# Optimization experiments

Hardware: AMD Instinct MI355X
Metric: run time of the kernel (lower is better)

The kernel has to match this reference:

```python
import jax, jax.numpy as jnp
import numpy as np

N_ITERS = 1000   # n_iters default
LR = 0.1         # SGD lr default (schedule_lr=False -> constant lr)
EPS = 1e-8       # eps in LogMagTargetFrequencyLoss


def setup_inputs() -> dict:
    key = jax.random.key(0)
    k1, k2 = jax.random.split(key)
    # random log-magnitude target in dB (scaled to plausible dB range)
    target_dB = jax.random.normal(k1, (512,), dtype=jnp.float32) * 6.0
    # matches torch.rand(1, 16, 6) init of self.coefs / self.sos
    sos_init = jax.random.uniform(k2, (1, 16, 6), dtype=jnp.float32)
    return {"target_dB": target_dB, "sos_init": sos_init}


def _log_mag_loss(sos, target):
    """LogMagTargetFrequencyLoss: MSE between 20*log10|H(e^jw)| of the SOS
    cascade and the target dB response. sos: (1,16,6); target: (1,N)."""
    n = target.shape[-1]
    w = jnp.linspace(0.0, jnp.pi, n)                      # frequency grid (N,)
    zm = jnp.exp(-1j * w.astype(jnp.complex64))            # z^-1 on unit circle
    powers = jnp.stack([jnp.ones_like(zm), zm, zm * zm])   # (3, N): [1, z^-1, z^-2]
    b = sos[..., :3].astype(jnp.complex64)                 # (1,16,3)
    a = sos[..., 3:].astype(jnp.complex64)                 # (1,16,3)
    num = jnp.einsum('bsc,cn->bsn', b, powers)             # (1,16,N)
    den = jnp.einsum('bsc,cn->bsn', a, powers)             # (1,16,N)
    h = jnp.prod(num / den, axis=1)                        # cascade product -> (1,N)
    mag = 20.0 * jnp.log10(jnp.abs(h) + EPS)
    return jnp.mean((mag - target) ** 2)


def reference(target_dB, sos_init):
    target = target_dB.reshape(1, -1)
    grad_fn = jax.grad(_log_mag_loss)

    def step(sos, _):
        g = grad_fn(sos, target)
        return sos - LR * g, None   # plain SGD, constant lr (schedule_lr=False)

    sos, _ = jax.lax.scan(step, sos_init, None, length=N_ITERS)
    # pole_zero=False: out_sos aliases self.sos, so the returned tensor is the
    # post-step (final optimized) coefficients.
    return sos
```

## Files before the change

kernel.cpp:

```cpp
#include <hip/hip_runtime.h>
#include <math.h>

#define NITER 1000
#define LRATE 0.1f

typedef unsigned int v2u __attribute__((ext_vector_type(2)));

__device__ __forceinline__ float rcpf(float x) { return __builtin_amdgcn_rcpf(x); }

__device__ __forceinline__ float readlane_f(float v, int l) {
    return __int_as_float(__builtin_amdgcn_readlane(__float_as_int(v), l));
}

template<int CTRL>
__device__ __forceinline__ float dpp_mov(float v) {
    return __int_as_float(__builtin_amdgcn_update_dpp(0, __float_as_int(v), CTRL, 0xF, 0xF, true));
}

__device__ __forceinline__ int lane_id() {
    return __builtin_amdgcn_mbcnt_hi(~0u, __builtin_amdgcn_mbcnt_lo(~0u, 0u));
}

__device__ __forceinline__ void swap16(float& x, float& y) {
#if __has_builtin(__builtin_amdgcn_permlane16_swap)
    v2u r = __builtin_amdgcn_permlane16_swap(__float_as_uint(x), __float_as_uint(y), false, false);
    x = __uint_as_float(r[0]);
    y = __uint_as_float(r[1]);
#else
    const bool up = lane_id() & 16;
    const float send = up ? x : y;
    const float recv = __shfl_xor(send, 16);
    x = up ? recv : x;
    y = up ? y : recv;
#endif
}

__device__ __forceinline__ void swap32(float& x, float& y) {
#if __has_builtin(__builtin_amdgcn_permlane32_swap)
    v2u r = __builtin_amdgcn_permlane32_swap(__float_as_uint(x), __float_as_uint(y), false, false);
    x = __uint_as_float(r[0]);
    y = __uint_as_float(r[1]);
#else
    const bool up = lane_id() & 32;
    const float send = up ? x : y;
    const float recv = __shfl_xor(send, 32);
    x = up ? recv : x;
    y = up ? y : recv;
#endif
}

__global__ __launch_bounds__(1024, 1)
void sgd_filter_design_kernel(const float* __restrict__ target,
                              const float* __restrict__ sos_init,
                              float* __restrict__ out)
{
    const int t = threadIdx.x;
    const int w = t >> 6;
    const int L = t & 63;

    __shared__ __align__(16) float wq[16][576];
    __shared__ __align__(16) float Kbuf[576];

    const float PI = 3.14159265358979323846f;
    float C1[8], S1[8], C2[8], S2[8];
    #pragma unroll
    for (int f = 0; f < 8; ++f) {
        const int n = 8 * L + f;
        const float wr = PI * (float)n / 511.0f;
        const float c1 = cosf(wr), s1 = sinf(wr);
        C1[f] = c1; S1[f] = s1;
        C2[f] = 2.0f * c1 * c1 - 1.0f;
        S2[f] = 2.0f * s1 * c1;
    }

    float mKt = 0.0f;
    int kaddr = 0;
    if (t < 512) {
        mKt = -0.03392925639869154f * target[t];
        kaddr = 8 * (t >> 3) + 4 * (t >> 5) + (t & 7);
    }

    const int sw = 8 * L + 4 * (L >> 2);
    const int col = ((L & 16) >> 2) | ((L & 32) >> 4) | (L & 1);
    const bool up1 = L & 1;

    float v0 = 0.0f;
    if (col < 6) v0 = sos_init[6 * w + col];
    float B0f = readlane_f(v0, 0);
    float B1f = readlane_f(v0, 1);
    float B2f = readlane_f(v0, 32);
    float A0f = readlane_f(v0, 33);
    float A1f = readlane_f(v0, 16);
    float A2f = readlane_f(v0, 17);

    for (int it = 0; it < NITER; ++it) {
        float imn[8], imd[8], qs[8];
        #pragma unroll
        for (int f = 0; f < 8; ++f) {
            const float nr = fmaf(B2f, C2[f], fmaf(B1f, C1[f], B0f));
            const float ni = fmaf(B2f, S2[f], B1f * S1[f]);
            const float dr = fmaf(A2f, C2[f], fmaf(A1f, C1[f], A0f));
            const float di = fmaf(A2f, S2[f], A1f * S1[f]);
            const float mn = fmaf(nr, nr, ni * ni);
            const float md = fmaf(dr, dr, di * di);
            const float rr = rcpf(mn * md);
            const float iimd = rr * mn;
            const float iimn = rr * md;
            qs[f] = mn * iimd;
            imn[f] = iimn;
            imd[f] = iimd;
        }
        {
            const float4 q0 = {qs[0], qs[1], qs[2], qs[3]};
            const float4 q1 = {qs[4], qs[5], qs[6], qs[7]};
            *reinterpret_cast<float4*>(&wq[w][sw])     = q0;
            *reinterpret_cast<float4*>(&wq[w][sw + 4]) = q1;
        }
        __syncthreads();

        if (t < 512) {
            float p[16];
            #pragma unroll
            for (int ww = 0; ww < 16; ++ww) p[ww] = wq[ww][kaddr];
            p[0] *= p[8];  p[1] *= p[9];  p[2] *= p[10]; p[3] *= p[11];
            p[4] *= p[12]; p[5] *= p[13]; p[6] *= p[14]; p[7] *= p[15];
            p[0] *= p[4];  p[1] *= p[5];  p[2] *= p[6];  p[3] *= p[7];
            p[0] *= p[2];  p[1] *= p[3];
            p[0] *= p[1];
            Kbuf[kaddr] = fmaf(__log2f(p[0]), 0.10213724040f, mKt);
        }
        __syncthreads();

        const float4 k0 = *reinterpret_cast<const float4*>(&Kbuf[sw]);
        const float4 k1 = *reinterpret_cast<const float4*>(&Kbuf[sw + 4]);
        const float Kf[8] = {k0.x, k0.y, k0.z, k0.w, k1.x, k1.y, k1.z, k1.w};

        float X0, X1, X2, X3, X4, X5;
        #pragma unroll
        for (int f = 0; f < 8; ++f) {
            const float E = Kf[f] * imn[f];
            const float F = Kf[f] * imd[f];
            if (f == 0) {
                X0 = E;            X3 = F;
                X1 = E * C1[f];    X4 = F * C1[f];
                X2 = E * C2[f];    X5 = F * C2[f];
            } else {
                X0 += E;                      X3 += F;
                X1 = fmaf(E, C1[f], X1);      X4 = fmaf(F, C1[f], X4);
                X2 = fmaf(E, C2[f], X2);      X5 = fmaf(F, C2[f], X5);
            }
        }
        const float g6[6] = {X0, X1, X2, X3, X4, X5};

        float r4v[4];
        #pragma unroll
        for (int i = 0; i < 4; ++i) {
            float x = g6[i];
            float y = (i + 4 < 6) ? g6[i + 4] : 0.0f;
            swap16(x, y);
            r4v[i] = x + y;
        }
        float r2v[2];
        #pragma unroll
        for (int i = 0; i < 2; ++i) {
            float x = r4v[i], y = r4v[i + 2];
            swap32(x, y);
            r2v[i] = x + y;
        }
        float r1v;
        {
            const float x = r2v[0], y = r2v[1];
            const float P = up1 ? y : x, Q = up1 ? x : y;
            r1v = P + dpp_mov<0xB1>(Q);
        }
        r1v += dpp_mov<0x4E>(r1v);
        r1v += dpp_mov<0x128>(r1v);
        r1v += __shfl_xor(r1v, 4);

        const float S0 = readlane_f(r1v, 0);
        const float S1v = readlane_f(r1v, 1);
        const float S2v = readlane_f(r1v, 32);
        const float T0 = readlane_f(r1v, 33);
        const float T1v = readlane_f(r1v, 16);
        const float T2v = readlane_f(r1v, 17);

        const float gb0 = fmaf(B0f, S0, fmaf(B1f, S1v, B2f * S2v));
        const float gb1 = fmaf(B0f + B2f, S1v, B1f * S0);
        const float gb2 = fmaf(B0f, S2v, fmaf(B1f, S1v, B2f * S0));
        const float ga0 = fmaf(A0f, T0, fmaf(A1f, T1v, A2f * T2v));
        const float ga1 = fmaf(A0f + A2f, T1v, A1f * T0);
        const float ga2 = fmaf(A0f, T2v, fmaf(A1f, T1v, A2f * T0));

        B0f = fmaf(-LRATE, gb0, B0f);
        B1f = fmaf(-LRATE, gb1, B1f);
        B2f = fmaf(-LRATE, gb2, B2f);
        A0f = fmaf( LRATE, ga0, A0f);
        A1f = fmaf( LRATE, ga1, A1f);
        A2f = fmaf( LRATE, ga2, A2f);
    }

    if (L == 0) {
        out[6 * w + 0] = B0f;
        out[6 * w + 1] = B1f;
        out[6 * w + 2] = B2f;
        out[6 * w + 3] = A0f;
        out[6 * w + 4] = A1f;
        out[6 * w + 5] = A2f;
    }
}

extern "C" void kernel_launch(void* const* d_in, const int* in_sizes, int n_in,
                              void* d_out, int out_size, void* d_ws, size_t ws_size,
                              hipStream_t stream) {
    const float* target   = (const float*)d_in[0];
    const float* sos_init = (const float*)d_in[1];
    float* out = (float*)d_out;
    hipLaunchKernelGGL(sgd_filter_design_kernel, dim3(1), dim3(1024), 0, stream,
                       target, sos_init, out);
}
```

Measured before the change: 1.479 ms.

## Split cascade product across all 1024 threads and store K in fp16

The per-frequency product over 16 sections is now split between lane pairs: each thread multiplies 8 sections and a DPP swap combines the pair, so all 1024 threads take part instead of 512. The loss-gradient factor K is written to shared memory as fp16 with a linear index, so each lane reads its 8 values with a single 16-byte load. The q writes are also interleaved with the computation in two halves. The intent is a shorter critical path per iteration, but K loses precision in fp16, which may change the optimized coefficients over 1000 iterations.

```diff
diff --git a/kernel.cpp b/kernel.cpp
--- a/kernel.cpp
+++ b/kernel.cpp
@@ -59,7 +59,7 @@
     const int L = t & 63;
 
     __shared__ __align__(16) float wq[16][576];
-    __shared__ __align__(16) float Kbuf[576];
+    __shared__ __align__(16) __fp16 Kh[512];
 
     const float PI = 3.14159265358979323846f;
     float C1[8], S1[8], C2[8], S2[8];
@@ -73,12 +73,10 @@
         S2[f] = 2.0f * s1 * c1;
     }
 
-    float mKt = 0.0f;
-    int kaddr = 0;
-    if (t < 512) {
-        mKt = -0.03392925639869154f * target[t];
-        kaddr = 8 * (t >> 3) + 4 * (t >> 5) + (t & 7);
-    }
+    const int fK = t >> 1;
+    const float mKt = -0.03392925639869154f * target[fK];
+    const int kaddr = 8 * (fK >> 3) + 4 * (fK >> 5) + (fK & 7);
+    const int wbase = (L & 1) ? 8 : 0;
 
     const int sw = 8 * L + 4 * (L >> 2);
     const int col = ((L & 16) >> 2) | ((L & 32) >> 4) | (L & 1);
@@ -94,46 +92,59 @@
     float A2f = readlane_f(v0, 17);
 
     for (int it = 0; it < NITER; ++it) {
-        float imn[8], imd[8], qs[8];
-        #pragma unroll
-        for (int f = 0; f < 8; ++f) {
-            const float nr = fmaf(B2f, C2[f], fmaf(B1f, C1[f], B0f));
-            const float ni = fmaf(B2f, S2[f], B1f * S1[f]);
-            const float dr = fmaf(A2f, C2[f], fmaf(A1f, C1[f], A0f));
-            const float di = fmaf(A2f, S2[f], A1f * S1[f]);
-            const float mn = fmaf(nr, nr, ni * ni);
-            const float md = fmaf(dr, dr, di * di);
-            const float rr = rcpf(mn * md);
-            const float iimd = rr * mn;
-            const float iimn = rr * md;
-            qs[f] = mn * iimd;
-            imn[f] = iimn;
-            imd[f] = iimd;
-        }
+        float imn[8], imd[8];
+        #pragma unroll
+        for (int half = 0; half < 2; ++half) {
+            float4 qv;
+            #pragma unroll
+            for (int j = 0; j < 4; ++j) {
+                const int f = 4 * half + j;
+                const float nr = fmaf(B2f, C2[f], fmaf(B1f, C1[f], B0f));
+                const float ni = fmaf(B2f, S2[f], B1f * S1[f]);
+                const float dr = fmaf(A2f, C2[f], fmaf(A1f, C1[f], A0f));
+                const float di = fmaf(A2f, S2[f], A1f * S1[f]);
+                const float mn = fmaf(nr, nr, ni * ni);
+                const float md = fmaf(dr, dr, di * di);
+                const float rr = rcpf(mn * md);
+                const float iimd = rr * mn;
+                const float iimn = rr * md;
+                imn[f] = iimn;
+                imd[f] = iimd;
+                const float q = mn * iimd;
+                if (j == 0) qv.x = q;
+                else if (j == 1) qv.y = q;
+                else if (j == 2) qv.z = q;
+                else qv.w = q;
+            }
+            *reinterpret_cast<float4*>(&wq[w][sw + 4 * half]) = qv;
+        }
+        __syncthreads();
+
         {
-            const float4 q0 = {qs[0], qs[1], qs[2], qs[3]};
-            const float4 q1 = {qs[4], qs[5], qs[6], qs[7]};
-            *reinterpret_cast<float4*>(&wq[w][sw])     = q0;
-            *reinterpret_cast<float4*>(&wq[w][sw + 4]) = q1;
+            float p0 = wq[wbase + 0][kaddr];
+            float p1 = wq[wbase + 1][kaddr];
+            float p2 = wq[wbase + 2][kaddr];
+            float p3 = wq[wbase + 3][kaddr];
+            const float p4 = wq[wbase + 4][kaddr];
+            const float p5 = wq[wbase + 5][kaddr];
+            const float p6 = wq[wbase + 6][kaddr];
+            const float p7 = wq[wbase + 7][kaddr];
+            p0 *= p4; p1 *= p5; p2 *= p6; p3 *= p7;
+            p0 *= p2; p1 *= p3;
+            p0 *= p1;
+            const float ptot = p0 * dpp_mov<0xB1>(p0);
+            const float Kv = fmaf(__log2f(ptot), 0.10213724040f, mKt);
+            if (!(L & 1)) Kh[fK] = (__fp16)Kv;
         }
         __syncthreads();
 
-        if (t < 512) {
-            float p[16];
+        float Kf[8];
+        {
+            union { uint4 u; __fp16 h[8]; } kc;
+            kc.u = *reinterpret_cast<const uint4*>(&Kh[8 * L]);
             #pragma unroll
-            for (int ww = 0; ww < 16; ++ww) p[ww] = wq[ww][kaddr];
-            p[0] *= p[8];  p[1] *= p[9];  p[2] *= p[10]; p[3] *= p[11];
-            p[4] *= p[12]; p[5] *= p[13]; p[6] *= p[14]; p[7] *= p[15];
-            p[0] *= p[4];  p[1] *= p[5];  p[2] *= p[6];  p[3] *= p[7];
-            p[0] *= p[2];  p[1] *= p[3];
-            p[0] *= p[1];
-            Kbuf[kaddr] = fmaf(__log2f(p[0]), 0.10213724040f, mKt);
-        }
-        __syncthreads();
-
-        const float4 k0 = *reinterpret_cast<const float4*>(&Kbuf[sw]);
-        const float4 k1 = *reinterpret_cast<const float4*>(&Kbuf[sw + 4]);
-        const float Kf[8] = {k0.x, k0.y, k0.z, k0.w, k1.x, k1.y, k1.z, k1.w};
+            for (int f = 0; f < 8; ++f) Kf[f] = (float)kc.h[f];
+        }
 
         float X0, X1, X2, X3, X4, X5;
         #pragma unroll
```

After: 1.991 ms. 1.35x slower.

## Pack two SOS sections per wave and use real-polynomial squared magnitudes

Applied to the files above, without the earlier changes.

The squared magnitudes |N|^2 and |D|^2 are now computed as real cosine polynomials (P0 + P1 cos w + P2 cos 2w) from per-section coefficients, so the complex evaluation and the sine tables go away. Each wave now handles two biquad sections, which halves the block to 512 threads and 8 waves. The cross-wave product reduction uses 8 instead of 16 loads, and all threads take part. This cuts barrier participants and per-iteration ALU work, at the cost of more registers per thread and a clamp with fmaxf that slightly changes numerics near zeros.

```diff
diff --git a/kernel.cpp b/kernel.cpp
--- a/kernel.cpp
+++ b/kernel.cpp
@@ -49,7 +49,7 @@
 #endif
 }
 
-__global__ __launch_bounds__(1024, 1)
+__global__ __launch_bounds__(512, 1)
 void sgd_filter_design_kernel(const float* __restrict__ target,
                               const float* __restrict__ sos_init,
                               float* __restrict__ out)
@@ -58,57 +58,72 @@
     const int w = t >> 6;
     const int L = t & 63;
 
-    __shared__ __align__(16) float wq[16][576];
+    __shared__ __align__(16) float wq[8][576];
     __shared__ __align__(16) float Kbuf[576];
 
     const float PI = 3.14159265358979323846f;
-    float C1[8], S1[8], C2[8], S2[8];
+    float C1[8], C2[8];
     #pragma unroll
     for (int f = 0; f < 8; ++f) {
         const int n = 8 * L + f;
         const float wr = PI * (float)n / 511.0f;
-        const float c1 = cosf(wr), s1 = sinf(wr);
-        C1[f] = c1; S1[f] = s1;
+        const float c1 = cosf(wr);
+        C1[f] = c1;
         C2[f] = 2.0f * c1 * c1 - 1.0f;
-        S2[f] = 2.0f * s1 * c1;
     }
 
-    float mKt = 0.0f;
-    int kaddr = 0;
-    if (t < 512) {
-        mKt = -0.03392925639869154f * target[t];
-        kaddr = 8 * (t >> 3) + 4 * (t >> 5) + (t & 7);
-    }
-
+    const float mKt = -0.03392925639869154f * target[t];
+    const int kaddr = 8 * (t >> 3) + 4 * (t >> 5) + (t & 7);
     const int sw = 8 * L + 4 * (L >> 2);
-    const int col = ((L & 16) >> 2) | ((L & 32) >> 4) | (L & 1);
-    const bool up1 = L & 1;
+
+    const int col = ((L & 16) >> 1) | ((L & 32) >> 3) | ((L & 1) << 1) | ((L & 2) >> 1);
+    const bool up1 = L & 1, up2 = L & 2;
 
     float v0 = 0.0f;
-    if (col < 6) v0 = sos_init[6 * w + col];
-    float B0f = readlane_f(v0, 0);
-    float B1f = readlane_f(v0, 1);
-    float B2f = readlane_f(v0, 32);
-    float A0f = readlane_f(v0, 33);
-    float A1f = readlane_f(v0, 16);
-    float A2f = readlane_f(v0, 17);
+    if (col < 12) v0 = sos_init[12 * w + col];
+    float b0A = readlane_f(v0, 0);
+    float b1A = readlane_f(v0, 2);
+    float b2A = readlane_f(v0, 1);
+    float a0A = readlane_f(v0, 3);
+    float a1A = readlane_f(v0, 32);
+    float a2A = readlane_f(v0, 34);
+    float b0B = readlane_f(v0, 33);
+    float b1B = readlane_f(v0, 35);
+    float b2B = readlane_f(v0, 16);
+    float a0B = readlane_f(v0, 18);
+    float a1B = readlane_f(v0, 17);
+    float a2B = readlane_f(v0, 19);
 
     for (int it = 0; it < NITER; ++it) {
-        float imn[8], imd[8], qs[8];
+        const float PA0 = fmaf(b0A, b0A, fmaf(b1A, b1A, b2A * b2A));
+        const float PA1 = 2.0f * b1A * (b0A + b2A);
+        const float PA2 = 2.0f * b0A * b2A;
+        const float QA0 = fmaf(a0A, a0A, fmaf(a1A, a1A, a2A * a2A));
+        const float QA1 = 2.0f * a1A * (a0A + a2A);
+        const float QA2 = 2.0f * a0A * a2A;
+        const float PB0 = fmaf(b0B, b0B, fmaf(b1B, b1B, b2B * b2B));
+        const float PB1 = 2.0f * b1B * (b0B + b2B);
+        const float PB2 = 2.0f * b0B * b2B;
+        const float QB0 = fmaf(a0B, a0B, fmaf(a1B, a1B, a2B * a2B));
+        const float QB1 = 2.0f * a1B * (a0B + a2B);
+        const float QB2 = 2.0f * a0B * a2B;
+
+        float imnA[8], imdA[8], imnB[8], imdB[8], qs[8];
         #pragma unroll
         for (int f = 0; f < 8; ++f) {
-            const float nr = fmaf(B2f, C2[f], fmaf(B1f, C1[f], B0f));
-            const float ni = fmaf(B2f, S2[f], B1f * S1[f]);
-            const float dr = fmaf(A2f, C2[f], fmaf(A1f, C1[f], A0f));
-            const float di = fmaf(A2f, S2[f], A1f * S1[f]);
-            const float mn = fmaf(nr, nr, ni * ni);
-            const float md = fmaf(dr, dr, di * di);
-            const float rr = rcpf(mn * md);
-            const float iimd = rr * mn;
-            const float iimn = rr * md;
-            qs[f] = mn * iimd;
-            imn[f] = iimn;
-            imd[f] = iimd;
+            float mnA = fmaf(PA2, C2[f], fmaf(PA1, C1[f], PA0));
+            float mdA = fmaf(QA2, C2[f], fmaf(QA1, C1[f], QA0));
+            float mnB = fmaf(PB2, C2[f], fmaf(PB1, C1[f], PB0));
+            float mdB = fmaf(QB2, C2[f], fmaf(QB1, C1[f], QB0));
+            mnA = fmaxf(mnA, 1e-18f);
+            mdA = fmaxf(mdA, 1e-18f);
+            mnB = fmaxf(mnB, 1e-18f);
+            mdB = fmaxf(mdB, 1e-18f);
+            const float rA = rcpf(mnA * mdA);
+            const float rB = rcpf(mnB * mdB);
+            imnA[f] = rA * mdA; imdA[f] = rA * mnA;
+            imnB[f] = rB * mdB; imdB[f] = rB * mnB;
+            qs[f] = (mnA * imdA[f]) * (mnB * imdB[f]);
         }
         {
             const float4 q0 = {qs[0], qs[1], qs[2], qs[3]};
@@ -118,16 +133,15 @@
         }
         __syncthreads();
 
-        if (t < 512) {
-            float p[16];
-            #pragma unroll
-            for (int ww = 0; ww < 16; ++ww) p[ww] = wq[ww][kaddr];
-            p[0] *= p[8];  p[1] *= p[9];  p[2] *= p[10]; p[3] *= p[11];
-            p[4] *= p[12]; p[5] *= p[13]; p[6] *= p[14]; p[7] *= p[15];
-            p[0] *= p[4];  p[1] *= p[5];  p[2] *= p[6];  p[3] *= p[7];
-            p[0] *= p[2];  p[1] *= p[3];
-            p[0] *= p[1];
-            Kbuf[kaddr] = fmaf(__log2f(p[0]), 0.10213724040f, mKt);
+        {
+            float p0 = wq[0][kaddr], p1 = wq[1][kaddr];
+            float p2 = wq[2][kaddr], p3 = wq[3][kaddr];
+            const float p4 = wq[4][kaddr], p5 = wq[5][kaddr];
+            const float p6 = wq[6][kaddr], p7 = wq[7][kaddr];
+            p0 *= p4; p1 *= p5; p2 *= p6; p3 *= p7;
+            p0 *= p2; p1 *= p3;
+            p0 *= p1;
+            Kbuf[kaddr] = fmaf(__log2f(p0), 0.10213724040f, mKt);
         }
         __syncthreads();
 
@@ -135,77 +149,117 @@
         const float4 k1 = *reinterpret_cast<const float4*>(&Kbuf[sw + 4]);
         const float Kf[8] = {k0.x, k0.y, k0.z, k0.w, k1.x, k1.y, k1.z, k1.w};
 
-        float X0, X1, X2, X3, X4, X5;
+        float SA0, SA1, SA2, TA0, TA1, TA2;
+        float SB0, SB1, SB2, TB0, TB1, TB2;
         #pragma unroll
         for (int f = 0; f < 8; ++f) {
-            const float E = Kf[f] * imn[f];
-            const float F = Kf[f] * imd[f];
+            const float EA = Kf[f] * imnA[f];
+            const float FA = Kf[f] * imdA[f];
+            const float EB = Kf[f] * imnB[f];
+            const float FB = Kf[f] * imdB[f];
             if (f == 0) {
-                X0 = E;            X3 = F;
-                X1 = E * C1[f];    X4 = F * C1[f];
-                X2 = E * C2[f];    X5 = F * C2[f];
+                SA0 = EA;          TA0 = FA;
+                SA1 = EA * C1[f];  TA1 = FA * C1[f];
+                SA2 = EA * C2[f];  TA2 = FA * C2[f];
+                SB0 = EB;          TB0 = FB;
+                SB1 = EB * C1[f];  TB1 = FB * C1[f];
+                SB2 = EB * C2[f];  TB2 = FB * C2[f];
             } else {
-                X0 += E;                      X3 += F;
-                X1 = fmaf(E, C1[f], X1);      X4 = fmaf(F, C1[f], X4);
-                X2 = fmaf(E, C2[f], X2);      X5 = fmaf(F, C2[f], X5);
+                SA0 += EA;                    TA0 += FA;
+                SA1 = fmaf(EA, C1[f], SA1);   TA1 = fmaf(FA, C1[f], TA1);
+                SA2 = fmaf(EA, C2[f], SA2);   TA2 = fmaf(FA, C2[f], TA2);
+                SB0 += EB;                    TB0 += FB;
+                SB1 = fmaf(EB, C1[f], SB1);   TB1 = fmaf(FB, C1[f], TB1);
+                SB2 = fmaf(EB, C2[f], SB2);   TB2 = fmaf(FB, C2[f], TB2);
             }
         }
-        const float g6[6] = {X0, X1, X2, X3, X4, X5};
-
+        const float g12[12] = {SA0, SA1, SA2, TA0, TA1, TA2,
+                               SB0, SB1, SB2, TB0, TB1, TB2};
+
+        float r8v[8];
+        #pragma unroll
+        for (int i = 0; i < 8; ++i) {
+            float x = g12[i];
+            float y = (i + 8 < 12) ? g12[i + 8] : 0.0f;
+            swap16(x, y);
+            r8v[i] = x + y;
+        }
         float r4v[4];
         #pragma unroll
         for (int i = 0; i < 4; ++i) {
-            float x = g6[i];
-            float y = (i + 4 < 6) ? g6[i + 4] : 0.0f;
-            swap16(x, y);
+            float x = r8v[i], y = r8v[i + 4];
+            swap32(x, y);
             r4v[i] = x + y;
         }
         float r2v[2];
         #pragma unroll
         for (int i = 0; i < 2; ++i) {
-            float x = r4v[i], y = r4v[i + 2];
-            swap32(x, y);
-            r2v[i] = x + y;
+            const float x = r4v[i], y = r4v[i + 2];
+            const float P = up1 ? y : x, Q = up1 ? x : y;
+            r2v[i] = P + dpp_mov<0xB1>(Q);
         }
         float r1v;
         {
             const float x = r2v[0], y = r2v[1];
-            const float P = up1 ? y : x, Q = up1 ? x : y;
-            r1v = P + dpp_mov<0xB1>(Q);
-        }
-        r1v += dpp_mov<0x4E>(r1v);
+            const float P = up2 ? y : x, Q = up2 ? x : y;
+            r1v = P + dpp_mov<0x4E>(Q);
+        }
         r1v += dpp_mov<0x128>(r1v);
         r1v += __shfl_xor(r1v, 4);
 
-        const float S0 = readlane_f(r1v, 0);
-        const float S1v = readlane_f(r1v, 1);
-        const float S2v = readlane_f(r1v, 32);
-        const float T0 = readlane_f(r1v, 33);
-        const float T1v = readlane_f(r1v, 16);
-        const float T2v = readlane_f(r1v, 17);
-
-        const float gb0 = fmaf(B0f, S0, fmaf(B1f, S1v, B2f * S2v));
-        const float gb1 = fmaf(B0f + B2f, S1v, B1f * S0);
-        const float gb2 = fmaf(B0f, S2v, fmaf(B1f, S1v, B2f * S0));
-        const float ga0 = fmaf(A0f, T0, fmaf(A1f, T1v, A2f * T2v));
-        const float ga1 = fmaf(A0f + A2f, T1v, A1f * T0);
-        const float ga2 = fmaf(A0f, T2v, fmaf(A1f, T1v, A2f * T0));
-
-        B0f = fmaf(-LRATE, gb0, B0f);
-        B1f = fmaf(-LRATE, gb1, B1f);
-        B2f = fmaf(-LRATE, gb2, B2f);
-        A0f = fmaf( LRATE, ga0, A0f);
-        A1f = fmaf( LRATE, ga1, A1f);
-        A2f = fmaf( LRATE, ga2, A2f);
+        const float sSA0 = readlane_f(r1v, 0);
+        const float sSA1 = readlane_f(r1v, 2);
+        const float sSA2 = readlane_f(r1v, 1);
+        const float sTA0 = readlane_f(r1v, 3);
+        const float sTA1 = readlane_f(r1v, 32);
+        const float sTA2 = readlane_f(r1v, 34);
+        const float sSB0 = readlane_f(r1v, 33);
+        const float sSB1 = readlane_f(r1v, 35);
+        const float sSB2 = readlane_f(r1v, 16);
+        const float sTB0 = readlane_f(r1v, 18);
+        const float sTB1 = readlane_f(r1v, 17);
+        const float sTB2 = readlane_f(r1v, 19);
+
+        const float gb0A = fmaf(b0A, sSA0, fmaf(b1A, sSA1, b2A * sSA2));
+        const float gb1A = fmaf(b0A + b2A, sSA1, b1A * sSA0);
+        const float gb2A = fmaf(b0A, sSA2, fmaf(b1A, sSA1, b2A * sSA0));
+        const float ga0A = fmaf(a0A, sTA0, fmaf(a1A, sTA1, a2A * sTA2));
+        const float ga1A = fmaf(a0A + a2A, sTA1, a1A * sTA0);
+        const float ga2A = fmaf(a0A, sTA2, fmaf(a1A, sTA1, a2A * sTA0));
+        const float gb0B = fmaf(b0B, sSB0, fmaf(b1B, sSB1, b2B * sSB2));
+        const float gb1B = fmaf(b0B + b2B, sSB1, b1B * sSB0);
+        const float gb2B = fmaf(b0B, sSB2, fmaf(b1B, sSB1, b2B * sSB0));
+        const float ga0B = fmaf(a0B, sTB0, fmaf(a1B, sTB1, a2B * sTB2));
+        const float ga1B = fmaf(a0B + a2B, sTB1, a1B * sTB0);
+        const float ga2B = fmaf(a0B, sTB2, fmaf(a1B, sTB1, a2B * sTB0));
+
+        b0A = fmaf(-LRATE, gb0A, b0A);
+        b1A = fmaf(-LRATE, gb1A, b1A);
+        b2A = fmaf(-LRATE, gb2A, b2A);
+        a0A = fmaf( LRATE, ga0A, a0A);
+        a1A = fmaf( LRATE, ga1A, a1A);
+        a2A = fmaf( LRATE, ga2A, a2A);
+        b0B = fmaf(-LRATE, gb0B, b0B);
+        b1B = fmaf(-LRATE, gb1B, b1B);
+        b2B = fmaf(-LRATE, gb2B, b2B);
+        a0B = fmaf( LRATE, ga0B, a0B);
+        a1B = fmaf( LRATE, ga1B, a1B);
+        a2B = fmaf( LRATE, ga2B, a2B);
     }
 
     if (L == 0) {
-        out[6 * w + 0] = B0f;
-        out[6 * w + 1] = B1f;
-        out[6 * w + 2] = B2f;
-        out[6 * w + 3] = A0f;
-        out[6 * w + 4] = A1f;
-        out[6 * w + 5] = A2f;
+        out[12 * w + 0]  = b0A;
+        out[12 * w + 1]  = b1A;
+        out[12 * w + 2]  = b2A;
+        out[12 * w + 3]  = a0A;
+        out[12 * w + 4]  = a1A;
+        out[12 * w + 5]  = a2A;
+        out[12 * w + 6]  = b0B;
+        out[12 * w + 7]  = b1B;
+        out[12 * w + 8]  = b2B;
+        out[12 * w + 9]  = a0B;
+        out[12 * w + 10] = a1B;
+        out[12 * w + 11] = a2B;
     }
 }
 
@@ -215,6 +269,6 @@
     const float* target   = (const float*)d_in[0];
     const float* sos_init = (const float*)d_in[1];
     float* out = (float*)d_out;
-    hipLaunchKernelGGL(sgd_filter_design_kernel, dim3(1), dim3(1024), 0, stream,
+    hipLaunchKernelGGL(sgd_filter_design_kernel, dim3(1), dim3(512), 0, stream,
                        target, sos_init, out);
 }
```

Measured after the change: 1.529 ms. 1.03x slower.
